# Performance work log

Measured on AMD Instinct MI355X. Metric: run time of the kernel, lower is better.

Reference implementation:

```python
import jax, jax.numpy as jnp
import numpy as np

N, L0, L1, D = 8, 128, 256, 512
NEG_INF = 1e12


def setup_inputs() -> dict:
    key = jax.random.key(0)
    k = jax.random.split(key, 7)
    x = jax.random.normal(k[0], (N, L0, D), dtype=jnp.float32)
    m = jax.random.normal(k[1], (N, L1, D), dtype=jnp.float32)
    mask = jax.random.randint(k[2], (N, L1), 0, 2, dtype=jnp.int32)
    # Linear(2D -> D): weight [D, 2D], bias [D]; Linear(D -> 1): weight [1, D], bias [1]
    s1 = 1.0 / np.sqrt(2 * D)
    W_w = jax.random.uniform(k[3], (D, 2 * D), jnp.float32, -s1, s1)
    W_b = jax.random.uniform(k[4], (D,), jnp.float32, -s1, s1)
    s2 = 1.0 / np.sqrt(D)
    V_w = jax.random.uniform(k[5], (1, D), jnp.float32, -s2, s2)
    V_b = jax.random.uniform(k[6], (1,), jnp.float32, -s2, s2)
    return {"x": x, "m": m, "mask": mask, "W_w": W_w, "W_b": W_b, "V_w": V_w, "V_b": V_b}


def reference(x, m, mask, W_w, W_b, V_w, V_b):
    # Split W so we never materialize the [N,L0,L1,2D] concat:
    # W([x_c, m_c]) == x @ Wx^T + m @ Wm^T (broadcast-added)
    Wx, Wm = W_w[:, :D], W_w[:, D:]
    xp = jnp.einsum('nld,ed->nle', x, Wx)           # [N,L0,D]
    mp = jnp.einsum('nld,ed->nle', m, Wm)           # [N,L1,D]
    h = jnp.tanh(xp[:, :, None, :] + mp[:, None, :, :] + W_b)  # [N,L0,L1,D]
    w = jnp.einsum('nabd,d->nab', h, V_w[0]) + V_b[0]           # [N,L0,L1]
    w = jnp.where((mask == 0)[:, None, :], -NEG_INF, w)
    w = jax.nn.softmax(w, axis=-1)
    v = jnp.einsum('nab,nbd->nad', w, m)            # sum_b w * m_c
    return v
```

## Files before the change

### kernel.cpp

```cpp
#include <hip/hip_runtime.h>
#include <hip/hip_bf16.h>

#define DD 512
#define NN 8
#define LL0 128
#define LL1 256

#define LOG2E2 2.8853900817779268f

#define PSTR ((size_t)3072 * 512)

typedef float f32x4 __attribute__((ext_vector_type(4)));
typedef __bf16 bf16x8 __attribute__((ext_vector_type(8)));

__device__ __forceinline__ float fexp2(float x) {
#if __has_builtin(__builtin_amdgcn_exp2f)
    return __builtin_amdgcn_exp2f(x);
#else
    float r; asm("v_exp_f32 %0, %1" : "=v"(r) : "v"(x)); return r;
#endif
}
__device__ __forceinline__ float frcp(float x) {
#if __has_builtin(__builtin_amdgcn_rcpf)
    return __builtin_amdgcn_rcpf(x);
#else
    float r; asm("v_rcp_f32 %0, %1" : "=v"(r) : "v"(x)); return r;
#endif
}

__device__ __forceinline__ unsigned short f2bf(float f) {
    unsigned int u = __float_as_uint(f);
    u += 0x7fffu + ((u >> 16) & 1u);
    return (unsigned short)(u >> 16);
}

__global__ __launch_bounds__(256) void cvt_kernel(
    const float* __restrict__ x, const float* __restrict__ m,
    const float* __restrict__ W,
    unsigned short* __restrict__ A16, unsigned short* __restrict__ W16)
{
    size_t i4 = ((size_t)blockIdx.x * 256 + threadIdx.x) * 4;
    const float* src;
    unsigned short* dst;
    if (i4 < (size_t)3072 * 512) {
        src = (i4 < (size_t)1024 * 512) ? x + i4 : m + (i4 - (size_t)1024 * 512);
        dst = A16 + i4;
    } else {
        size_t j = i4 - (size_t)3072 * 512;
        src = W + j; dst = W16 + j;
    }
    float4 v = *(const float4*)src;
    ushort4 o = make_ushort4(f2bf(v.x), f2bf(v.y), f2bf(v.z), f2bf(v.w));
    *(ushort4*)dst = o;
}

__global__ __launch_bounds__(256, 3) void mfma_proj_kernel(
    const unsigned short* __restrict__ A16, const unsigned short* __restrict__ W16,
    float* __restrict__ pp)
{
    __shared__ unsigned short As[64][68];
    __shared__ unsigned short Bs[64][68];

    int e0   = blockIdx.x * 64;
    int row0 = blockIdx.y * 64;
    int kb0  = blockIdx.z * 256;
    bool isx = row0 < (NN * LL0);
    int koff = isx ? 0 : DD;

    int tid  = threadIdx.x;
    int wid  = tid >> 6;
    int lane = tid & 63;
    int l15  = lane & 15, lk = lane >> 4;

    int srow = tid >> 2;
    int scol = (tid & 3) * 16;

    const unsigned short* Ap = A16 + (size_t)(row0 + srow) * DD + kb0 + scol;
    const unsigned short* Bp = W16 + (size_t)(e0 + srow) * (2 * DD) + koff + kb0 + scol;

    uint4 a0 = *(const uint4*)(Ap);
    uint4 a1 = *(const uint4*)(Ap + 8);
    uint4 b0 = *(const uint4*)(Bp);
    uint4 b1 = *(const uint4*)(Bp + 8);

    f32x4 acc[4] = {};

    for (int kt = 0; kt < 4; ++kt) {
        if (kt) __syncthreads();
        *(uint2*)&As[srow][scol + 0]  = make_uint2(a0.x, a0.y);
        *(uint2*)&As[srow][scol + 4]  = make_uint2(a0.z, a0.w);
        *(uint2*)&As[srow][scol + 8]  = make_uint2(a1.x, a1.y);
        *(uint2*)&As[srow][scol + 12] = make_uint2(a1.z, a1.w);
        *(uint2*)&Bs[srow][scol + 0]  = make_uint2(b0.x, b0.y);
        *(uint2*)&Bs[srow][scol + 4]  = make_uint2(b0.z, b0.w);
        *(uint2*)&Bs[srow][scol + 8]  = make_uint2(b1.x, b1.y);
        *(uint2*)&Bs[srow][scol + 12] = make_uint2(b1.z, b1.w);
        if (kt < 3) {
            int ko = (kt + 1) * 64;
            a0 = *(const uint4*)(Ap + ko);
            a1 = *(const uint4*)(Ap + ko + 8);
            b0 = *(const uint4*)(Bp + ko);
            b1 = *(const uint4*)(Bp + ko + 8);
        }
        __syncthreads();

        #pragma unroll
        for (int kb = 0; kb < 2; ++kb) {
            union { unsigned int u[4]; bf16x8 v; } af;
            {
                const uint2* p = (const uint2*)&As[wid * 16 + l15][kb * 32 + lk * 8];
                uint2 lo = p[0], hi = p[1];
                af.u[0] = lo.x; af.u[1] = lo.y; af.u[2] = hi.x; af.u[3] = hi.y;
            }
            #pragma unroll
            for (int ni = 0; ni < 4; ++ni) {
                union { unsigned int u[4]; bf16x8 v; } bf;
                const uint2* p = (const uint2*)&Bs[ni * 16 + l15][kb * 32 + lk * 8];
                uint2 lo = p[0], hi = p[1];
                bf.u[0] = lo.x; bf.u[1] = lo.y; bf.u[2] = hi.x; bf.u[3] = hi.y;
                acc[ni] = __builtin_amdgcn_mfma_f32_16x16x32_bf16(af.v, bf.v, acc[ni], 0, 0, 0);
            }
        }
    }

    float* outp = pp + (size_t)blockIdx.z * PSTR;
    #pragma unroll
    for (int ni = 0; ni < 4; ++ni) {
        int col = e0 + ni * 16 + l15;
        #pragma unroll
        for (int r = 0; r < 4; ++r) {
            int row = row0 + wid * 16 + lk * 4 + r;
            outp[(size_t)row * DD + col] = acc[ni][r];
        }
    }
}

__global__ __launch_bounds__(256, 3) void logits_kernel(
    const float* __restrict__ pp, const float* __restrict__ Wb,
    const float* __restrict__ Vw, float* __restrict__ wpart)
{
    __shared__ __attribute__((aligned(16))) float xs[64][34];
    __shared__ __attribute__((aligned(16))) float ms[64][68];
    __shared__ __attribute__((aligned(16))) float vsh[64];

    int n  = blockIdx.z;
    int bt = blockIdx.x;
    int at = blockIdx.y & 3;
    int dc = blockIdx.y >> 2;
    int tid = threadIdx.x;
    int ty = tid >> 4, tx = tid & 15;

    {
        int r  = tid & 31;
        int c8 = (tid >> 5) * 8;
        size_t base = ((size_t)(n * LL0 + at * 32) + r) * DD + dc * 64 + c8;
        float4 p00 = *(const float4*)(pp + base);
        float4 p01 = *(const float4*)(pp + base + 4);
        float4 p10 = *(const float4*)(pp + PSTR + base);
        float4 p11 = *(const float4*)(pp + PSTR + base + 4);
        float4 w0  = *(const float4*)(Wb + dc * 64 + c8);
        float4 w1  = *(const float4*)(Wb + dc * 64 + c8 + 4);
        xs[c8 + 0][r] = fexp2(LOG2E2 * (p00.x + p10.x + w0.x));
        xs[c8 + 1][r] = fexp2(LOG2E2 * (p00.y + p10.y + w0.y));
        xs[c8 + 2][r] = fexp2(LOG2E2 * (p00.z + p10.z + w0.z));
        xs[c8 + 3][r] = fexp2(LOG2E2 * (p00.w + p10.w + w0.w));
        xs[c8 + 4][r] = fexp2(LOG2E2 * (p01.x + p11.x + w1.x));
        xs[c8 + 5][r] = fexp2(LOG2E2 * (p01.y + p11.y + w1.y));
        xs[c8 + 6][r] = fexp2(LOG2E2 * (p01.z + p11.z + w1.z));
        xs[c8 + 7][r] = fexp2(LOG2E2 * (p01.w + p11.w + w1.w));
    }
    {
        int r   = tid & 63;
        int c16 = (tid >> 6) * 16;
        size_t base = ((size_t)(NN * LL0 + n * LL1 + bt * 64) + r) * DD
                      + dc * 64 + c16;
        #pragma unroll
        for (int q = 0; q < 4; ++q) {
            float4 p0 = *(const float4*)(pp + base + q * 4);
            float4 p1 = *(const float4*)(pp + PSTR + base + q * 4);
            int c = c16 + q * 4;
            ms[c + 0][r] = fexp2(LOG2E2 * (p0.x + p1.x));
            ms[c + 1][r] = fexp2(LOG2E2 * (p0.y + p1.y));
            ms[c + 2][r] = fexp2(LOG2E2 * (p0.z + p1.z));
            ms[c + 3][r] = fexp2(LOG2E2 * (p0.w + p1.w));
        }
        if (tid < 16)
            *(float4*)&vsh[tid * 4] = *(const float4*)(Vw + dc * 64 + tid * 4);
    }
    __syncthreads();

    float acc[2][4] = {};

    #pragma unroll 4
    for (int kk = 0; kk < 64; kk += 4) {
        float2 xa0 = *(const float2*)&xs[kk + 0][ty * 2];
        float2 xa1 = *(const float2*)&xs[kk + 1][ty * 2];
        float2 xa2 = *(const float2*)&xs[kk + 2][ty * 2];
        float2 xa3 = *(const float2*)&xs[kk + 3][ty * 2];
        float4 mb0 = *(const float4*)&ms[kk + 0][tx * 4];
        float4 mb1 = *(const float4*)&ms[kk + 1][tx * 4];
        float4 mb2 = *(const float4*)&ms[kk + 2][tx * 4];
        float4 mb3 = *(const float4*)&ms[kk + 3][tx * 4];
        float4 vv  = *(const float4*)&vsh[kk];

        float ex[4][2] = {{xa0.x, xa0.y}, {xa1.x, xa1.y},
                          {xa2.x, xa2.y}, {xa3.x, xa3.y}};
        float fm[4][4] = {{mb0.x, mb0.y, mb0.z, mb0.w},
                          {mb1.x, mb1.y, mb1.z, mb1.w},
                          {mb2.x, mb2.y, mb2.z, mb2.w},
                          {mb3.x, mb3.y, mb3.z, mb3.w}};
        #pragma unroll
        for (int i = 0; i < 2; ++i) {
            #pragma unroll
            for (int j = 0; j < 4; ++j) {
                float D0 = fmaf(ex[0][i], fm[0][j], 1.0f);
                float D1 = fmaf(ex[1][i], fm[1][j], 1.0f);
                float D2 = fmaf(ex[2][i], fm[2][j], 1.0f);
                float D3 = fmaf(ex[3][i], fm[3][j], 1.0f);
                float P01 = D0 * D1, P23 = D2 * D3;
                float N01 = fmaf(vv.x, D1, vv.y * D0);
                float N23 = fmaf(vv.z, D3, vv.w * D2);
                float N   = fmaf(N01, P23, N23 * P01);
                acc[i][j] = fmaf(N, frcp(P01 * P23), acc[i][j]);
            }
        }
    }

    const size_t P = (size_t)NN * LL0 * LL1;
    float* wp = wpart + (size_t)dc * P
              + ((size_t)n * LL0 + at * 32 + ty * 2) * LL1 + bt * 64 + tx * 4;
    *(float4*)(wp)       = make_float4(acc[0][0], acc[0][1], acc[0][2], acc[0][3]);
    *(float4*)(wp + LL1) = make_float4(acc[1][0], acc[1][1], acc[1][2], acc[1][3]);
}

__global__ __launch_bounds__(256) void softmax_kernel(
    float* __restrict__ wpart, const int* __restrict__ mask)
{
    __shared__ float red2[4];
    const size_t P = (size_t)NN * LL0 * LL1;
    int row = blockIdx.x;
    int n = row >> 7;
    int b = threadIdx.x;
    size_t idx = (size_t)row * LL1 + b;

    float s8 = 0.f;
    #pragma unroll
    for (int p = 0; p < 8; ++p) s8 += wpart[idx + (size_t)p * P];
    float w = -2.0f * s8;

    float e = (mask[n * LL1 + b] != 0) ? __expf(w) : 0.f;
    float s = e;
    #pragma unroll
    for (int off = 32; off; off >>= 1) s += __shfl_xor(s, off);
    int wv = threadIdx.x >> 6;
    if ((threadIdx.x & 63) == 0) red2[wv] = s;
    __syncthreads();
    s = red2[0] + red2[1] + red2[2] + red2[3];

    wpart[idx] = e / s;
}

__global__ __launch_bounds__(256, 4) void vgemm_kernel(
    const float* __restrict__ wbuf, const float* __restrict__ m,
    float* __restrict__ out)
{
    __shared__ float wt[32][36];
    __shared__ float mt[32][68];

    int n  = blockIdx.z;
    int a0 = blockIdx.y * 32;
    int d0 = blockIdx.x * 64;
    int tid = threadIdx.x;
    int ty = tid >> 4, tx = tid & 15;

    const float* wrow = wbuf + ((size_t)n * LL0 + a0) * LL1;
    const float* mrow = m + (size_t)n * LL1 * DD;

    float acc[2][4] = {};
    for (int k0 = 0; k0 < LL1; k0 += 32) {
        {
            int r  = tid >> 3;
            int c4 = (tid & 7) * 4;
            float4 wv = *(const float4*)(wrow + (size_t)r * LL1 + k0 + c4);
            wt[c4 + 0][r] = wv.x; wt[c4 + 1][r] = wv.y;
            wt[c4 + 2][r] = wv.z; wt[c4 + 3][r] = wv.w;
        }
        {
            int r  = tid >> 3;
            int c8 = (tid & 7) * 8;
            const float* src = mrow + (size_t)(k0 + r) * DD + d0 + c8;
            *(float4*)&mt[r][c8]     = *(const float4*)(src);
            *(float4*)&mt[r][c8 + 4] = *(const float4*)(src + 4);
        }
        __syncthreads();
        #pragma unroll 8
        for (int kk = 0; kk < 32; ++kk) {
            float2 av = *(const float2*)&wt[kk][ty * 2];
            float4 bv = *(const float4*)&mt[kk][tx * 4];
            acc[0][0] = fmaf(av.x, bv.x, acc[0][0]);
            acc[0][1] = fmaf(av.x, bv.y, acc[0][1]);
            acc[0][2] = fmaf(av.x, bv.z, acc[0][2]);
            acc[0][3] = fmaf(av.x, bv.w, acc[0][3]);
            acc[1][0] = fmaf(av.y, bv.x, acc[1][0]);
            acc[1][1] = fmaf(av.y, bv.y, acc[1][1]);
            acc[1][2] = fmaf(av.y, bv.z, acc[1][2]);
            acc[1][3] = fmaf(av.y, bv.w, acc[1][3]);
        }
        __syncthreads();
    }
    float* op = out + ((size_t)n * LL0 + a0 + ty * 2) * DD + d0 + tx * 4;
    *(float4*)(op)      = make_float4(acc[0][0], acc[0][1], acc[0][2], acc[0][3]);
    *(float4*)(op + DD) = make_float4(acc[1][0], acc[1][1], acc[1][2], acc[1][3]);
}

extern "C" void kernel_launch(void* const* d_in, const int* in_sizes, int n_in,
                              void* d_out, int out_size, void* d_ws, size_t ws_size,
                              hipStream_t stream) {
    const float* x    = (const float*)d_in[0];
    const float* m    = (const float*)d_in[1];
    const int*   mask = (const int*)d_in[2];
    const float* W_w  = (const float*)d_in[3];
    const float* W_b  = (const float*)d_in[4];
    const float* V_w  = (const float*)d_in[5];
    const float* V_b  = (const float*)d_in[6];
    (void)V_b;
    float* out = (float*)d_out;

    float* pp    = (float*)d_ws;
    float* wpart = pp + 2 * PSTR;
    unsigned short* A16 = (unsigned short*)(wpart + (size_t)8 * NN * LL0 * LL1);
    unsigned short* W16 = A16 + (size_t)3072 * 512;

    cvt_kernel<<<dim3(2048), 256, 0, stream>>>(x, m, W_w, A16, W16);
    mfma_proj_kernel<<<dim3(8, 48, 2), 256, 0, stream>>>(A16, W16, pp);
    logits_kernel<<<dim3(4, 32, 8), 256, 0, stream>>>(pp, W_b, V_w, wpart);
    softmax_kernel<<<dim3(1024), 256, 0, stream>>>(wpart, mask);
    vgemm_kernel<<<dim3(8, 4, 8), 256, 0, stream>>>(wpart, m, out);
}
```

Baseline: 49.33 us.

## Fuse softmax into PV GEMM with deferred normalization

```diff
diff --git a/kernel.cpp b/kernel.cpp
--- a/kernel.cpp
+++ b/kernel.cpp
@@ -233,58 +233,60 @@
     *(float4*)(wp + LL1) = make_float4(acc[1][0], acc[1][1], acc[1][2], acc[1][3]);
 }
 
-__global__ __launch_bounds__(256) void softmax_kernel(
-    float* __restrict__ wpart, const int* __restrict__ mask)
+__global__ __launch_bounds__(256, 3) void pv_kernel(
+    const float* __restrict__ wpart, const int* __restrict__ mask,
+    const float* __restrict__ m, float* __restrict__ out)
 {
-    __shared__ float red2[4];
+    __shared__ float wt[256][36];
+    __shared__ float mt[32][68];
+    __shared__ float rsum[32][9];
+    __shared__ float rinv[32];
+
     const size_t P = (size_t)NN * LL0 * LL1;
-    int row = blockIdx.x;
-    int n = row >> 7;
-    int b = threadIdx.x;
-    size_t idx = (size_t)row * LL1 + b;
-
-    float s8 = 0.f;
-    #pragma unroll
-    for (int p = 0; p < 8; ++p) s8 += wpart[idx + (size_t)p * P];
-    float w = -2.0f * s8;
-
-    float e = (mask[n * LL1 + b] != 0) ? __expf(w) : 0.f;
-    float s = e;
-    #pragma unroll
-    for (int off = 32; off; off >>= 1) s += __shfl_xor(s, off);
-    int wv = threadIdx.x >> 6;
-    if ((threadIdx.x & 63) == 0) red2[wv] = s;
-    __syncthreads();
-    s = red2[0] + red2[1] + red2[2] + red2[3];
-
-    wpart[idx] = e / s;
-}
-
-__global__ __launch_bounds__(256, 4) void vgemm_kernel(
-    const float* __restrict__ wbuf, const float* __restrict__ m,
-    float* __restrict__ out)
-{
-    __shared__ float wt[32][36];
-    __shared__ float mt[32][68];
-
     int n  = blockIdx.z;
     int a0 = blockIdx.y * 32;
     int d0 = blockIdx.x * 64;
     int tid = threadIdx.x;
     int ty = tid >> 4, tx = tid & 15;
 
-    const float* wrow = wbuf + ((size_t)n * LL0 + a0) * LL1;
+    {
+        int a = tid & 31;
+        int g = tid >> 5;
+        const float* wp0 = wpart + ((size_t)(n * LL0) + a0 + a) * LL1 + g * 32;
+        const int*   mk  = mask + n * LL1 + g * 32;
+        float ls = 0.f;
+        #pragma unroll
+        for (int q = 0; q < 8; ++q) {
+            float4 s4 = make_float4(0.f, 0.f, 0.f, 0.f);
+            #pragma unroll
+            for (int p = 0; p < 8; ++p) {
+                float4 pv = *(const float4*)(wp0 + (size_t)p * P + q * 4);
+                s4.x += pv.x; s4.y += pv.y; s4.z += pv.z; s4.w += pv.w;
+            }
+            int4 mv = *(const int4*)(mk + q * 4);
+            float w0 = mv.x ? __expf(-2.f * s4.x) : 0.f;
+            float w1 = mv.y ? __expf(-2.f * s4.y) : 0.f;
+            float w2 = mv.z ? __expf(-2.f * s4.z) : 0.f;
+            float w3 = mv.w ? __expf(-2.f * s4.w) : 0.f;
+            int b = g * 32 + q * 4;
+            wt[b + 0][a] = w0; wt[b + 1][a] = w1;
+            wt[b + 2][a] = w2; wt[b + 3][a] = w3;
+            ls += w0 + w1 + w2 + w3;
+        }
+        rsum[a][g] = ls;
+    }
+    __syncthreads();
+    if (tid < 32) {
+        float s = 0.f;
+        #pragma unroll
+        for (int g = 0; g < 8; ++g) s += rsum[tid][g];
+        rinv[tid] = frcp(s);
+    }
+    __syncthreads();
+
     const float* mrow = m + (size_t)n * LL1 * DD;
-
     float acc[2][4] = {};
     for (int k0 = 0; k0 < LL1; k0 += 32) {
-        {
-            int r  = tid >> 3;
-            int c4 = (tid & 7) * 4;
-            float4 wv = *(const float4*)(wrow + (size_t)r * LL1 + k0 + c4);
-            wt[c4 + 0][r] = wv.x; wt[c4 + 1][r] = wv.y;
-            wt[c4 + 2][r] = wv.z; wt[c4 + 3][r] = wv.w;
-        }
         {
             int r  = tid >> 3;
             int c8 = (tid & 7) * 8;
@@ -295,7 +297,7 @@
         __syncthreads();
         #pragma unroll 8
         for (int kk = 0; kk < 32; ++kk) {
-            float2 av = *(const float2*)&wt[kk][ty * 2];
+            float2 av = *(const float2*)&wt[k0 + kk][ty * 2];
             float4 bv = *(const float4*)&mt[kk][tx * 4];
             acc[0][0] = fmaf(av.x, bv.x, acc[0][0]);
             acc[0][1] = fmaf(av.x, bv.y, acc[0][1]);
@@ -308,9 +310,13 @@
         }
         __syncthreads();
     }
+
+    float r0 = rinv[ty * 2], r1 = rinv[ty * 2 + 1];
     float* op = out + ((size_t)n * LL0 + a0 + ty * 2) * DD + d0 + tx * 4;
-    *(float4*)(op)      = make_float4(acc[0][0], acc[0][1], acc[0][2], acc[0][3]);
-    *(float4*)(op + DD) = make_float4(acc[1][0], acc[1][1], acc[1][2], acc[1][3]);
+    *(float4*)(op)      = make_float4(acc[0][0] * r0, acc[0][1] * r0,
+                                      acc[0][2] * r0, acc[0][3] * r0);
+    *(float4*)(op + DD) = make_float4(acc[1][0] * r1, acc[1][1] * r1,
+                                      acc[1][2] * r1, acc[1][3] * r1);
 }
 
 extern "C" void kernel_launch(void* const* d_in, const int* in_sizes, int n_in,
@@ -334,6 +340,5 @@
     cvt_kernel<<<dim3(2048), 256, 0, stream>>>(x, m, W_w, A16, W16);
     mfma_proj_kernel<<<dim3(8, 48, 2), 256, 0, stream>>>(A16, W16, pp);
     logits_kernel<<<dim3(4, 32, 8), 256, 0, stream>>>(pp, W_b, V_w, wpart);
-    softmax_kernel<<<dim3(1024), 256, 0, stream>>>(wpart, mask);
-    vgemm_kernel<<<dim3(8, 4, 8), 256, 0, stream>>>(wpart, m, out);
-}
+    pv_kernel<<<dim3(8, 4, 8), 256, 0, stream>>>(wpart, mask, m, out);
+}
```

Measured after the change: 85.29 us. +72.9%, slower.
